# Performance work log

Hardware: AMD Instinct MI355X
Metric: run time of the kernel (lower is better)

## Reference

```python
import jax, jax.numpy as jnp
import numpy as np

B, N, XD = 4, 8192, 256   # batch, seq len, input/kv feature dim
F, H = 512, 8             # features, heads
D = F // H                # per-head dim = 64
EPS = 1e-6                # flax LayerNorm default epsilon


def _layer_norm(t, scale, bias):
    mu = jnp.mean(t, axis=-1, keepdims=True)
    var = jnp.mean(jnp.square(t - mu), axis=-1, keepdims=True)
    return (t - mu) * jax.lax.rsqrt(var + EPS) * scale + bias


def setup_inputs() -> dict:
    key = jax.random.key(0)
    ks = jax.random.split(key, 5)
    return {
        "x": jax.random.normal(ks[0], (B, N, XD), jnp.float32),
        "kv": jax.random.normal(ks[1], (B, N, XD), jnp.float32),
        # linen.initializers.normal(1/x_dim) / normal(1/h_dim)
        "Q": jax.random.normal(ks[2], (XD, F), jnp.float32) * (1.0 / XD),
        "K": jax.random.normal(ks[3], (XD, F), jnp.float32) * (1.0 / XD),
        "V": jax.random.normal(ks[4], (XD, F), jnp.float32) * (1.0 / XD),
        "log_scale": jnp.zeros((F,), jnp.float32),
        "ln_q_scale": jnp.ones((D,), jnp.float32),
        "ln_q_bias": jnp.zeros((D,), jnp.float32),
        "ln_k_scale": jnp.ones((D,), jnp.float32),
        "ln_k_bias": jnp.zeros((D,), jnp.float32),
        "ln_v_scale": jnp.ones((D,), jnp.float32),
        "ln_v_bias": jnp.zeros((D,), jnp.float32),
    }


def reference(x, kv, Q, K, V, log_scale,
              ln_q_scale, ln_q_bias, ln_k_scale, ln_k_bias, ln_v_scale, ln_v_bias):
    # QKV projections (value scaled by exp(log_scale) per feature)
    query = x @ Q                                    # [B, N, F]
    key = kv @ K                                     # [B, N, F]
    value = jnp.exp(log_scale) * (kv @ V)            # [B, N, F]
    # reshape exactly as the source module does
    q = query.reshape(B, H, -1, D)                   # [B, H, N, D]
    k = key.reshape(B, H, -1, D)
    v = value.reshape(B, H, -1, D)
    # per-head LayerNorm over the head dim (layer_norm=True)
    q = _layer_norm(q, ln_q_scale, ln_q_bias)
    k = _layer_norm(k, ln_k_scale, ln_k_bias)
    v = _layer_norm(v, ln_v_scale, ln_v_bias)
    # galerkin linear attention: Q @ (K^T V) / seq_len, no softmax, no NxN scores
    seq_len = k.shape[-2]
    ctx = jnp.einsum('bhnd,bhne->bhde', k, v)        # [B, H, D, D]
    out = jnp.einsum('bhnd,bhde->bhne', q, ctx) / seq_len
    return out.reshape(B, N, F)
```

## Files before the change

kernel.cpp:

```cpp
#include <hip/hip_runtime.h>
#include <stdint.h>

using f32x4  = __attribute__((ext_vector_type(4))) float;
using short8 = __attribute__((ext_vector_type(8))) short;
using u16x4  = __attribute__((ext_vector_type(4))) unsigned short;

#define MFMA(a, b, c) __builtin_amdgcn_mfma_f32_16x16x32_bf16((a), (b), (c), 0, 0, 0)

#define XDIM 256
#define FDIM 512
#define EPS  1e-6f

#define QT_OFF    0u
#define KT_OFF    262144u
#define VT_OFF    524288u
#define CTXT_OFF  786432u
#define PART_OFF  1048576u

static __device__ __forceinline__ unsigned short f2bf(float f) {
  unsigned u = __float_as_uint(f);
  unsigned r = u + 0x7FFFu + ((u >> 16) & 1u);
  return (unsigned short)(r >> 16);
}

static __device__ __forceinline__ void stage_a_full(const float* a_rows, int tid, char* Alds) {
  const int r = tid >> 2, cq = tid & 3;
  const float* src = a_rows + (size_t)r * XDIM + cq * 64;
  char* dst = Alds + r * 528 + cq * 128;
#pragma unroll
  for (int i = 0; i < 4; ++i) {
    float4 f0 = *(const float4*)(src + i * 16);
    float4 f1 = *(const float4*)(src + i * 16 + 4);
    float4 f2 = *(const float4*)(src + i * 16 + 8);
    float4 f3 = *(const float4*)(src + i * 16 + 12);
    short8 v0, v1;
    v0[0] = (short)f2bf(f0.x); v0[1] = (short)f2bf(f0.y);
    v0[2] = (short)f2bf(f0.z); v0[3] = (short)f2bf(f0.w);
    v0[4] = (short)f2bf(f1.x); v0[5] = (short)f2bf(f1.y);
    v0[6] = (short)f2bf(f1.z); v0[7] = (short)f2bf(f1.w);
    v1[0] = (short)f2bf(f2.x); v1[1] = (short)f2bf(f2.y);
    v1[2] = (short)f2bf(f2.z); v1[3] = (short)f2bf(f2.w);
    v1[4] = (short)f2bf(f3.x); v1[5] = (short)f2bf(f3.y);
    v1[6] = (short)f2bf(f3.z); v1[7] = (short)f2bf(f3.w);
    *(short8*)(dst + i * 32)      = v0;
    *(short8*)(dst + i * 32 + 16) = v1;
  }
}

static __device__ __forceinline__ void load_bphase(const char* base, int ks, int lr, int koff,
                                                   short8 b[8]) {
#pragma unroll
  for (int nt = 0; nt < 4; ++nt) {
    const char* r = base + (size_t)(nt * 16 + lr) * 512 + ks * 128 + koff;
    b[nt * 2]     = *(const short8*)(r);
    b[nt * 2 + 1] = *(const short8*)(r + 64);
  }
}

static __device__ __forceinline__ void chunk_layernorm(f32x4 acc[4][4], const float* sc,
                                                       const float* bs, int lane) {
  const int lr = lane & 15;
  float scl[4], bia[4];
#pragma unroll
  for (int nt = 0; nt < 4; ++nt) { scl[nt] = sc[nt * 16 + lr]; bia[nt] = bs[nt * 16 + lr]; }
#pragma unroll
  for (int mt = 0; mt < 4; ++mt) {
#pragma unroll
    for (int j = 0; j < 4; ++j) {
      float a0 = acc[mt][0][j], a1 = acc[mt][1][j], a2 = acc[mt][2][j], a3 = acc[mt][3][j];
      float s  = a0 + a1 + a2 + a3;
      float s2 = a0 * a0 + a1 * a1 + a2 * a2 + a3 * a3;
#pragma unroll
      for (int off = 1; off < 16; off <<= 1) {
        s  += __shfl_xor(s, off, 16);
        s2 += __shfl_xor(s2, off, 16);
      }
      const float mu  = s * (1.0f / 64.0f);
      const float var = s2 * (1.0f / 64.0f) - mu * mu;
      const float rs  = rsqrtf(var + EPS);
#pragma unroll
      for (int nt = 0; nt < 4; ++nt)
        acc[mt][nt][j] = (acc[mt][nt][j] - mu) * rs * scl[nt] + bia[nt];
    }
  }
}

__global__ void prep_weights_kernel(const float* __restrict__ Q, const float* __restrict__ K,
                                    const float* __restrict__ V, const float* __restrict__ ls,
                                    unsigned short* __restrict__ Qt, unsigned short* __restrict__ Kt,
                                    unsigned short* __restrict__ Vt) {
  const int flat = blockIdx.x * 256 + threadIdx.x;
  const int mat = flat >> 17;
  const int rem = flat & 131071;
  const int f = rem & 511;
  const int k = rem >> 9;
  if (mat == 0)      Qt[f * 256 + k] = f2bf(Q[k * 512 + f]);
  else if (mat == 1) Kt[f * 256 + k] = f2bf(K[k * 512 + f]);
  else               Vt[f * 256 + k] = f2bf(V[k * 512 + f] * expf(ls[f]));
}

__launch_bounds__(256, 2)
__global__ void kv_ctx_kernel(const float* __restrict__ kv,
                              const unsigned short* __restrict__ Kt,
                              const unsigned short* __restrict__ Vt,
                              const float* __restrict__ lnk_s, const float* __restrict__ lnk_b,
                              const float* __restrict__ lnv_s, const float* __restrict__ lnv_b,
                              float* __restrict__ partials) {
  __shared__ __align__(16) char smem[33792];

  const int tid = threadIdx.x, lane = tid & 63, w = tid >> 6;
  const int bid = blockIdx.x, rb = bid >> 1, nb = bid & 1;
  const int row0 = rb * 64;
  const int lr = lane & 15, lk = lane >> 4;
  const int koff = lk * 16;

  stage_a_full(kv + (size_t)row0 * XDIM, tid, smem);

  const f32x4 z4 = {0.f, 0.f, 0.f, 0.f};
  f32x4 acck[4][4], accv[4][4];
#pragma unroll
  for (int i = 0; i < 4; ++i)
#pragma unroll
    for (int j = 0; j < 4; ++j) { acck[i][j] = z4; accv[i][j] = z4; }

  const char* kbase = (const char*)Kt + (size_t)(nb * 256 + w * 64) * 512;
  const char* vbase = (const char*)Vt + (size_t)(nb * 256 + w * 64) * 512;

  short8 bufK[8], bufV[8];
  load_bphase(kbase, 0, lr, koff, bufK);
  load_bphase(vbase, 0, lr, koff, bufV);

  __syncthreads();

#pragma unroll
  for (int ks = 0; ks < 4; ++ks) {
    short8 a0[4], a1[4];
#pragma unroll
    for (int mt = 0; mt < 4; ++mt) {
      const char* ar = smem + (mt * 16 + lr) * 528 + ks * 128;
      a0[mt] = *(const short8*)(ar + koff);
      a1[mt] = *(const short8*)(ar + 64 + koff);
    }
#pragma unroll
    for (int mt = 0; mt < 4; ++mt)
#pragma unroll
      for (int nt = 0; nt < 4; ++nt) {
        acck[mt][nt] = MFMA(a0[mt], bufK[nt * 2],     acck[mt][nt]);
        acck[mt][nt] = MFMA(a1[mt], bufK[nt * 2 + 1], acck[mt][nt]);
      }
    if (ks < 3) load_bphase(kbase, ks + 1, lr, koff, bufK);
#pragma unroll
    for (int mt = 0; mt < 4; ++mt)
#pragma unroll
      for (int nt = 0; nt < 4; ++nt) {
        accv[mt][nt] = MFMA(a0[mt], bufV[nt * 2],     accv[mt][nt]);
        accv[mt][nt] = MFMA(a1[mt], bufV[nt * 2 + 1], accv[mt][nt]);
      }
    if (ks < 3) load_bphase(vbase, ks + 1, lr, koff, bufV);
  }

  chunk_layernorm(acck, lnk_s, lnk_b, lane);
  chunk_layernorm(accv, lnv_s, lnv_b, lane);

  char* knT = smem;
  char* vnT = smem + 16384;
  f32x4 cacc[4];
#pragma unroll
  for (int i = 0; i < 4; ++i) cacc[i] = z4;
  const int drow = w * 16 + lr;

#pragma unroll
  for (int half = 0; half < 2; ++half) {
    __syncthreads();
    if ((w >> 1) == half) {
      const int tb2 = (w & 1) * 128;
#pragma unroll
      for (int mt = 0; mt < 4; ++mt) {
        const int tb = tb2 + mt * 32 + lk * 8;
#pragma unroll
        for (int nt = 0; nt < 4; ++nt) {
          const int d = nt * 16 + lr;
          u16x4 pk, pv;
#pragma unroll
          for (int j = 0; j < 4; ++j) {
            pk[j] = f2bf(acck[mt][nt][j]);
            pv[j] = f2bf(accv[mt][nt][j]);
          }
          const int boff = d * 256 + (tb ^ ((d & 7) << 4));
          *(u16x4*)(knT + boff) = pk;
          *(u16x4*)(vnT + boff) = pv;
        }
      }
    }
    __syncthreads();
#pragma unroll
    for (int s = 0; s < 4; ++s) {
      const short8 a = *(const short8*)(knT + drow * 256 + ((s * 64 + koff) ^ ((drow & 7) << 4)));
#pragma unroll
      for (int nt = 0; nt < 4; ++nt) {
        const int e = nt * 16 + lr;
        const short8 b = *(const short8*)(vnT + e * 256 + ((s * 64 + koff) ^ ((e & 7) << 4)));
        cacc[nt] = MFMA(a, b, cacc[nt]);
      }
    }
  }

  float* pout = partials + (size_t)bid * 4096;
#pragma unroll
  for (int nt = 0; nt < 4; ++nt)
#pragma unroll
    for (int j = 0; j < 4; ++j)
      pout[(w * 16 + lk * 4 + j) * 64 + nt * 16 + lr] = cacc[nt][j];
}

__global__ void reduce_ctx_kernel(const float* __restrict__ partials,
                                  unsigned short* __restrict__ ctxTg) {
  const int bid = blockIdx.x, t = threadIdx.x;
  const int gg = bid >> 3, sl = bid & 7;
  const float* base = partials + (size_t)gg * 32 * 4096;
#pragma unroll
  for (int rep = 0; rep < 2; ++rep) {
    const int idx = sl * 512 + rep * 256 + t;
    float acc = 0.f;
#pragma unroll 8
    for (int p = 0; p < 32; ++p) acc += base[(size_t)p * 4096 + idx];
    const int d = idx >> 6, e = idx & 63;
    ctxTg[(size_t)gg * 4096 + e * 64 + d] = f2bf(acc * (1.0f / 8192.0f));
  }
}

__launch_bounds__(256, 2)
__global__ void q_out_kernel(const float* __restrict__ x, const unsigned short* __restrict__ Qt,
                             const unsigned short* __restrict__ ctxTg,
                             const float* __restrict__ lnq_s, const float* __restrict__ lnq_b,
                             float* __restrict__ out) {
  __shared__ __align__(16) char smem[43008];

  const int tid = threadIdx.x, lane = tid & 63, w = tid >> 6;
  const int bid = blockIdx.x, rb = bid >> 1, nb = bid & 1;
  const int row0 = rb * 64;
  const int g = row0 >> 10;
  const int lr = lane & 15, lk = lane >> 4;
  const int koff = lk * 16;
  char* ctxT = smem + 33792;

  stage_a_full(x + (size_t)row0 * XDIM, tid, smem);

  {
    const unsigned short* src = ctxTg + (size_t)g * 4096 + (tid >> 2) * 64 + (tid & 3) * 16;
    char* dst = ctxT + (tid >> 2) * 144 + (tid & 3) * 32;
    *(short8*)dst        = *(const short8*)(src);
    *(short8*)(dst + 16) = *(const short8*)(src + 8);
  }

  const f32x4 z4 = {0.f, 0.f, 0.f, 0.f};
  f32x4 acc[4][4];
#pragma unroll
  for (int i = 0; i < 4; ++i)
#pragma unroll
    for (int j = 0; j < 4; ++j) acc[i][j] = z4;

  const char* qbase = (const char*)Qt + (size_t)(nb * 256 + w * 64) * 512;

  short8 buf0[8], buf1[8];
  load_bphase(qbase, 0, lr, koff, buf0);

  __syncthreads();

#pragma unroll
  for (int ks = 0; ks < 4; ++ks) {
    if (ks == 0) load_bphase(qbase, 1, lr, koff, buf1);
    if (ks == 1) load_bphase(qbase, 2, lr, koff, buf0);
    if (ks == 2) load_bphase(qbase, 3, lr, koff, buf1);
    short8 a0[4], a1[4];
#pragma unroll
    for (int mt = 0; mt < 4; ++mt) {
      const char* ar = smem + (mt * 16 + lr) * 528 + ks * 128;
      a0[mt] = *(const short8*)(ar + koff);
      a1[mt] = *(const short8*)(ar + 64 + koff);
    }
#pragma unroll
    for (int mt = 0; mt < 4; ++mt)
#pragma unroll
      for (int nt = 0; nt < 4; ++nt) {
        if ((ks & 1) == 0) {
          acc[mt][nt] = MFMA(a0[mt], buf0[nt * 2],     acc[mt][nt]);
          acc[mt][nt] = MFMA(a1[mt], buf0[nt * 2 + 1], acc[mt][nt]);
        } else {
          acc[mt][nt] = MFMA(a0[mt], buf1[nt * 2],     acc[mt][nt]);
          acc[mt][nt] = MFMA(a1[mt], buf1[nt * 2 + 1], acc[mt][nt]);
        }
      }
  }

  chunk_layernorm(acc, lnq_s, lnq_b, lane);

  __syncthreads();

  char* A2 = smem + w * 8192;
#pragma unroll
  for (int mt = 0; mt < 4; ++mt)
#pragma unroll
    for (int j = 0; j < 4; ++j) {
      const int m = mt * 16 + lk * 4 + j;
      const int sw = (m & 7) << 4;
#pragma unroll
      for (int nt = 0; nt < 4; ++nt) {
        const int d = nt * 16 + lr;
        *(unsigned short*)(A2 + m * 128 + ((d * 2) ^ sw)) = f2bf(acc[mt][nt][j]);
      }
    }
  __syncthreads();

  f32x4 o[4][4];
#pragma unroll
  for (int i = 0; i < 4; ++i)
#pragma unroll
    for (int j = 0; j < 4; ++j) o[i][j] = z4;

#pragma unroll
  for (int s = 0; s < 2; ++s) {
    short8 a[4], b[4];
#pragma unroll
    for (int mt = 0; mt < 4; ++mt) {
      const int m = mt * 16 + lr;
      a[mt] = *(const short8*)(A2 + m * 128 + ((s * 64 + koff) ^ ((m & 7) << 4)));
    }
#pragma unroll
    for (int nt = 0; nt < 4; ++nt)
      b[nt] = *(const short8*)(ctxT + (nt * 16 + lr) * 144 + s * 64 + koff);
#pragma unroll
    for (int mt = 0; mt < 4; ++mt)
#pragma unroll
      for (int nt = 0; nt < 4; ++nt)
        o[mt][nt] = MFMA(a[mt], b[nt], o[mt][nt]);
  }

#pragma unroll
  for (int mt = 0; mt < 4; ++mt)
#pragma unroll
    for (int nt = 0; nt < 4; ++nt)
#pragma unroll
      for (int j = 0; j < 4; ++j) {
        const int n = mt * 16 + lk * 4 + j;
        out[(size_t)(row0 + n) * FDIM + nb * 256 + w * 64 + nt * 16 + lr] = o[mt][nt][j];
      }
}

extern "C" void kernel_launch(void* const* d_in, const int* in_sizes, int n_in,
                              void* d_out, int out_size, void* d_ws, size_t ws_size,
                              hipStream_t stream) {
  (void)in_sizes; (void)n_in; (void)out_size; (void)ws_size;
  const float* x     = (const float*)d_in[0];
  const float* kv    = (const float*)d_in[1];
  const float* Q     = (const float*)d_in[2];
  const float* K     = (const float*)d_in[3];
  const float* V     = (const float*)d_in[4];
  const float* ls    = (const float*)d_in[5];
  const float* lnq_s = (const float*)d_in[6];
  const float* lnq_b = (const float*)d_in[7];
  const float* lnk_s = (const float*)d_in[8];
  const float* lnk_b = (const float*)d_in[9];
  const float* lnv_s = (const float*)d_in[10];
  const float* lnv_b = (const float*)d_in[11];
  float* out = (float*)d_out;

  char* ws = (char*)d_ws;
  unsigned short* Qt   = (unsigned short*)(ws + QT_OFF);
  unsigned short* Kt   = (unsigned short*)(ws + KT_OFF);
  unsigned short* Vt   = (unsigned short*)(ws + VT_OFF);
  unsigned short* ctxT = (unsigned short*)(ws + CTXT_OFF);
  float* partials      = (float*)(ws + PART_OFF);

  prep_weights_kernel<<<1536, 256, 0, stream>>>(Q, K, V, ls, Qt, Kt, Vt);
  kv_ctx_kernel<<<1024, 256, 0, stream>>>(kv, Kt, Vt, lnk_s, lnk_b, lnv_s, lnv_b, partials);
  reduce_ctx_kernel<<<256, 256, 0, stream>>>(partials, ctxT);
  q_out_kernel<<<1024, 256, 0, stream>>>(x, Qt, ctxT, lnq_s, lnq_b, out);
}
```

Before: 109.9 us.

## Pre-convert kv to bf16, replace partial reduction with atomics, remap block order

kv is now converted to bf16 in a combined prep kernel, so kv_ctx reads A fragments straight from global memory without LDS staging or a barrier. The separate reduce kernel is removed. Each block instead atomically adds its context partial into a zeroed fp32 ctx buffer, and q_out scales and transposes it into LDS itself. Block-index remapping groups the two feature halves of nearby row blocks, likely for cache locality. In exchange this adds an extra bf16 round-trip of kv through memory, a memset, atomic contention, and non-deterministic summation order.

```diff
diff --git a/kernel.cpp b/kernel.cpp
--- a/kernel.cpp
+++ b/kernel.cpp
@@ -11,11 +11,11 @@
 #define FDIM 512
 #define EPS  1e-6f
 
-#define QT_OFF    0u
-#define KT_OFF    262144u
-#define VT_OFF    524288u
-#define CTXT_OFF  786432u
-#define PART_OFF  1048576u
+#define QT_OFF   0u
+#define KT_OFF   262144u
+#define VT_OFF   524288u
+#define CTX_OFF  786432u
+#define KVB_OFF  1310720u
 
 static __device__ __forceinline__ unsigned short f2bf(float f) {
   unsigned u = __float_as_uint(f);
@@ -23,16 +23,58 @@
   return (unsigned short)(r >> 16);
 }
 
-static __device__ __forceinline__ void stage_a_full(const float* a_rows, int tid, char* Alds) {
-  const int r = tid >> 2, cq = tid & 3;
-  const float* src = a_rows + (size_t)r * XDIM + cq * 64;
-  char* dst = Alds + r * 528 + cq * 128;
-#pragma unroll
-  for (int i = 0; i < 4; ++i) {
-    float4 f0 = *(const float4*)(src + i * 16);
-    float4 f1 = *(const float4*)(src + i * 16 + 4);
-    float4 f2 = *(const float4*)(src + i * 16 + 8);
-    float4 f3 = *(const float4*)(src + i * 16 + 12);
+static __device__ __forceinline__ void load_bphase(const char* base, int ks, int lr, int koff,
+                                                   short8 b[8]) {
+#pragma unroll
+  for (int nt = 0; nt < 4; ++nt) {
+    const char* r = base + (size_t)(nt * 16 + lr) * 512 + ks * 128 + koff;
+    b[nt * 2]     = *(const short8*)(r);
+    b[nt * 2 + 1] = *(const short8*)(r + 64);
+  }
+}
+
+static __device__ __forceinline__ void chunk_layernorm(f32x4 acc[4][4], const float* sc,
+                                                       const float* bs, int lane) {
+  const int lr = lane & 15;
+  float scl[4], bia[4];
+#pragma unroll
+  for (int nt = 0; nt < 4; ++nt) { scl[nt] = sc[nt * 16 + lr]; bia[nt] = bs[nt * 16 + lr]; }
+#pragma unroll
+  for (int mt = 0; mt < 4; ++mt) {
+#pragma unroll
+    for (int j = 0; j < 4; ++j) {
+      float a0 = acc[mt][0][j], a1 = acc[mt][1][j], a2 = acc[mt][2][j], a3 = acc[mt][3][j];
+      float s  = a0 + a1 + a2 + a3;
+      float s2 = a0 * a0 + a1 * a1 + a2 * a2 + a3 * a3;
+#pragma unroll
+      for (int off = 1; off < 16; off <<= 1) {
+        s  += __shfl_xor(s, off, 16);
+        s2 += __shfl_xor(s2, off, 16);
+      }
+      const float mu  = s * (1.0f / 64.0f);
+      const float var = s2 * (1.0f / 64.0f) - mu * mu;
+      const float rs  = rsqrtf(var + EPS);
+#pragma unroll
+      for (int nt = 0; nt < 4; ++nt)
+        acc[mt][nt][j] = (acc[mt][nt][j] - mu) * rs * scl[nt] + bia[nt];
+    }
+  }
+}
+
+__global__ void prep_kernel(const float* __restrict__ kv,
+                            const float* __restrict__ Q, const float* __restrict__ K,
+                            const float* __restrict__ V, const float* __restrict__ ls,
+                            unsigned short* __restrict__ kvb,
+                            unsigned short* __restrict__ Qt, unsigned short* __restrict__ Kt,
+                            unsigned short* __restrict__ Vt) {
+  const int bid = blockIdx.x, tid = threadIdx.x;
+  if (bid < 2048) {
+    const size_t base = ((size_t)bid * 256 + tid) * 16;
+    const float* src = kv + base;
+    float4 f0 = *(const float4*)(src);
+    float4 f1 = *(const float4*)(src + 4);
+    float4 f2 = *(const float4*)(src + 8);
+    float4 f3 = *(const float4*)(src + 12);
     short8 v0, v1;
     v0[0] = (short)f2bf(f0.x); v0[1] = (short)f2bf(f0.y);
     v0[2] = (short)f2bf(f0.z); v0[3] = (short)f2bf(f0.w);
@@ -42,80 +84,38 @@
     v1[2] = (short)f2bf(f2.z); v1[3] = (short)f2bf(f2.w);
     v1[4] = (short)f2bf(f3.x); v1[5] = (short)f2bf(f3.y);
     v1[6] = (short)f2bf(f3.z); v1[7] = (short)f2bf(f3.w);
-    *(short8*)(dst + i * 32)      = v0;
-    *(short8*)(dst + i * 32 + 16) = v1;
-  }
-}
-
-static __device__ __forceinline__ void load_bphase(const char* base, int ks, int lr, int koff,
-                                                   short8 b[8]) {
-#pragma unroll
-  for (int nt = 0; nt < 4; ++nt) {
-    const char* r = base + (size_t)(nt * 16 + lr) * 512 + ks * 128 + koff;
-    b[nt * 2]     = *(const short8*)(r);
-    b[nt * 2 + 1] = *(const short8*)(r + 64);
-  }
-}
-
-static __device__ __forceinline__ void chunk_layernorm(f32x4 acc[4][4], const float* sc,
-                                                       const float* bs, int lane) {
-  const int lr = lane & 15;
-  float scl[4], bia[4];
-#pragma unroll
-  for (int nt = 0; nt < 4; ++nt) { scl[nt] = sc[nt * 16 + lr]; bia[nt] = bs[nt * 16 + lr]; }
-#pragma unroll
-  for (int mt = 0; mt < 4; ++mt) {
-#pragma unroll
-    for (int j = 0; j < 4; ++j) {
-      float a0 = acc[mt][0][j], a1 = acc[mt][1][j], a2 = acc[mt][2][j], a3 = acc[mt][3][j];
-      float s  = a0 + a1 + a2 + a3;
-      float s2 = a0 * a0 + a1 * a1 + a2 * a2 + a3 * a3;
-#pragma unroll
-      for (int off = 1; off < 16; off <<= 1) {
-        s  += __shfl_xor(s, off, 16);
-        s2 += __shfl_xor(s2, off, 16);
-      }
-      const float mu  = s * (1.0f / 64.0f);
-      const float var = s2 * (1.0f / 64.0f) - mu * mu;
-      const float rs  = rsqrtf(var + EPS);
-#pragma unroll
-      for (int nt = 0; nt < 4; ++nt)
-        acc[mt][nt][j] = (acc[mt][nt][j] - mu) * rs * scl[nt] + bia[nt];
-    }
-  }
-}
-
-__global__ void prep_weights_kernel(const float* __restrict__ Q, const float* __restrict__ K,
-                                    const float* __restrict__ V, const float* __restrict__ ls,
-                                    unsigned short* __restrict__ Qt, unsigned short* __restrict__ Kt,
-                                    unsigned short* __restrict__ Vt) {
-  const int flat = blockIdx.x * 256 + threadIdx.x;
-  const int mat = flat >> 17;
-  const int rem = flat & 131071;
-  const int f = rem & 511;
-  const int k = rem >> 9;
-  if (mat == 0)      Qt[f * 256 + k] = f2bf(Q[k * 512 + f]);
-  else if (mat == 1) Kt[f * 256 + k] = f2bf(K[k * 512 + f]);
-  else               Vt[f * 256 + k] = f2bf(V[k * 512 + f] * expf(ls[f]));
+    *(short8*)(kvb + base)     = v0;
+    *(short8*)(kvb + base + 8) = v1;
+  } else {
+    const int flat = (bid - 2048) * 256 + tid;
+    const int mat = flat >> 17;
+    const int rem = flat & 131071;
+    const int f = rem & 511;
+    const int k = rem >> 9;
+    if (mat == 0)      Qt[f * 256 + k] = f2bf(Q[k * 512 + f]);
+    else if (mat == 1) Kt[f * 256 + k] = f2bf(K[k * 512 + f]);
+    else               Vt[f * 256 + k] = f2bf(V[k * 512 + f] * expf(ls[f]));
+  }
 }
 
 __launch_bounds__(256, 2)
-__global__ void kv_ctx_kernel(const float* __restrict__ kv,
+__global__ void kv_ctx_kernel(const unsigned short* __restrict__ kvb,
                               const unsigned short* __restrict__ Kt,
                               const unsigned short* __restrict__ Vt,
                               const float* __restrict__ lnk_s, const float* __restrict__ lnk_b,
                               const float* __restrict__ lnv_s, const float* __restrict__ lnv_b,
-                              float* __restrict__ partials) {
-  __shared__ __align__(16) char smem[33792];
+                              float* __restrict__ ctx) {
+  __shared__ __align__(16) char smem[32768];
 
   const int tid = threadIdx.x, lane = tid & 63, w = tid >> 6;
-  const int bid = blockIdx.x, rb = bid >> 1, nb = bid & 1;
+  const int bid = blockIdx.x;
+  const int rb = ((bid >> 4) << 3) | (bid & 7);
+  const int nb = (bid >> 3) & 1;
   const int row0 = rb * 64;
+  const int g = row0 >> 10;
   const int lr = lane & 15, lk = lane >> 4;
   const int koff = lk * 16;
 
-  stage_a_full(kv + (size_t)row0 * XDIM, tid, smem);
-
   const f32x4 z4 = {0.f, 0.f, 0.f, 0.f};
   f32x4 acck[4][4], accv[4][4];
 #pragma unroll
@@ -123,6 +123,7 @@
 #pragma unroll
     for (int j = 0; j < 4; ++j) { acck[i][j] = z4; accv[i][j] = z4; }
 
+  const char* abase = (const char*)kvb + (size_t)row0 * 512;
   const char* kbase = (const char*)Kt + (size_t)(nb * 256 + w * 64) * 512;
   const char* vbase = (const char*)Vt + (size_t)(nb * 256 + w * 64) * 512;
 
@@ -130,16 +131,14 @@
   load_bphase(kbase, 0, lr, koff, bufK);
   load_bphase(vbase, 0, lr, koff, bufV);
 
-  __syncthreads();
-
 #pragma unroll
   for (int ks = 0; ks < 4; ++ks) {
     short8 a0[4], a1[4];
 #pragma unroll
     for (int mt = 0; mt < 4; ++mt) {
-      const char* ar = smem + (mt * 16 + lr) * 528 + ks * 128;
-      a0[mt] = *(const short8*)(ar + koff);
-      a1[mt] = *(const short8*)(ar + 64 + koff);
+      const char* ar = abase + (size_t)(mt * 16 + lr) * 512 + ks * 128 + koff;
+      a0[mt] = *(const short8*)(ar);
+      a1[mt] = *(const short8*)(ar + 64);
     }
 #pragma unroll
     for (int mt = 0; mt < 4; ++mt)
@@ -205,52 +204,63 @@
     }
   }
 
-  float* pout = partials + (size_t)bid * 4096;
+  float* cdst = ctx + (size_t)g * 4096;
 #pragma unroll
   for (int nt = 0; nt < 4; ++nt)
 #pragma unroll
     for (int j = 0; j < 4; ++j)
-      pout[(w * 16 + lk * 4 + j) * 64 + nt * 16 + lr] = cacc[nt][j];
-}
-
-__global__ void reduce_ctx_kernel(const float* __restrict__ partials,
-                                  unsigned short* __restrict__ ctxTg) {
-  const int bid = blockIdx.x, t = threadIdx.x;
-  const int gg = bid >> 3, sl = bid & 7;
-  const float* base = partials + (size_t)gg * 32 * 4096;
-#pragma unroll
-  for (int rep = 0; rep < 2; ++rep) {
-    const int idx = sl * 512 + rep * 256 + t;
-    float acc = 0.f;
-#pragma unroll 8
-    for (int p = 0; p < 32; ++p) acc += base[(size_t)p * 4096 + idx];
-    const int d = idx >> 6, e = idx & 63;
-    ctxTg[(size_t)gg * 4096 + e * 64 + d] = f2bf(acc * (1.0f / 8192.0f));
-  }
+      atomicAdd(cdst + (w * 16 + lk * 4 + j) * 64 + nt * 16 + lr, cacc[nt][j]);
 }
 
 __launch_bounds__(256, 2)
 __global__ void q_out_kernel(const float* __restrict__ x, const unsigned short* __restrict__ Qt,
-                             const unsigned short* __restrict__ ctxTg,
+                             const float* __restrict__ ctx,
                              const float* __restrict__ lnq_s, const float* __restrict__ lnq_b,
                              float* __restrict__ out) {
   __shared__ __align__(16) char smem[43008];
 
   const int tid = threadIdx.x, lane = tid & 63, w = tid >> 6;
-  const int bid = blockIdx.x, rb = bid >> 1, nb = bid & 1;
+  const int bid = blockIdx.x;
+  const int rb = ((bid >> 4) << 3) | (bid & 7);
+  const int nb = (bid >> 3) & 1;
   const int row0 = rb * 64;
   const int g = row0 >> 10;
   const int lr = lane & 15, lk = lane >> 4;
   const int koff = lk * 16;
   char* ctxT = smem + 33792;
 
-  stage_a_full(x + (size_t)row0 * XDIM, tid, smem);
-
   {
-    const unsigned short* src = ctxTg + (size_t)g * 4096 + (tid >> 2) * 64 + (tid & 3) * 16;
-    char* dst = ctxT + (tid >> 2) * 144 + (tid & 3) * 32;
-    *(short8*)dst        = *(const short8*)(src);
-    *(short8*)(dst + 16) = *(const short8*)(src + 8);
+    const int r = tid >> 2, cq = tid & 3;
+    const float* src = x + (size_t)(row0 + r) * XDIM + cq * 64;
+    char* dst = smem + r * 528 + cq * 128;
+#pragma unroll
+    for (int i = 0; i < 4; ++i) {
+      float4 f0 = *(const float4*)(src + i * 16);
+      float4 f1 = *(const float4*)(src + i * 16 + 4);
+      float4 f2 = *(const float4*)(src + i * 16 + 8);
+      float4 f3 = *(const float4*)(src + i * 16 + 12);
+      short8 v0, v1;
+      v0[0] = (short)f2bf(f0.x); v0[1] = (short)f2bf(f0.y);
+      v0[2] = (short)f2bf(f0.z); v0[3] = (short)f2bf(f0.w);
+      v0[4] = (short)f2bf(f1.x); v0[5] = (short)f2bf(f1.y);
+      v0[6] = (short)f2bf(f1.z); v0[7] = (short)f2bf(f1.w);
+      v1[0] = (short)f2bf(f2.x); v1[1] = (short)f2bf(f2.y);
+      v1[2] = (short)f2bf(f2.z); v1[3] = (short)f2bf(f2.w);
+      v1[4] = (short)f2bf(f3.x); v1[5] = (short)f2bf(f3.y);
+      v1[6] = (short)f2bf(f3.z); v1[7] = (short)f2bf(f3.w);
+      *(short8*)(dst + i * 32)      = v0;
+      *(short8*)(dst + i * 32 + 16) = v1;
+    }
+  }
+
+  {
+    const int d = tid >> 2, e0 = (tid & 3) * 16;
+    const float* csrc = ctx + (size_t)g * 4096 + d * 64 + e0;
+#pragma unroll
+    for (int i = 0; i < 16; ++i) {
+      const unsigned short v = f2bf(csrc[i] * (1.0f / 8192.0f));
+      *(unsigned short*)(ctxT + (e0 + i) * 144 + d * 2) = v;
+    }
   }
 
   const f32x4 z4 = {0.f, 0.f, 0.f, 0.f};
@@ -366,14 +376,14 @@
   float* out = (float*)d_out;
 
   char* ws = (char*)d_ws;
-  unsigned short* Qt   = (unsigned short*)(ws + QT_OFF);
-  unsigned short* Kt   = (unsigned short*)(ws + KT_OFF);
-  unsigned short* Vt   = (unsigned short*)(ws + VT_OFF);
-  unsigned short* ctxT = (unsigned short*)(ws + CTXT_OFF);
-  float* partials      = (float*)(ws + PART_OFF);
-
-  prep_weights_kernel<<<1536, 256, 0, stream>>>(Q, K, V, ls, Qt, Kt, Vt);
-  kv_ctx_kernel<<<1024, 256, 0, stream>>>(kv, Kt, Vt, lnk_s, lnk_b, lnv_s, lnv_b, partials);
-  reduce_ctx_kernel<<<256, 256, 0, stream>>>(partials, ctxT);
-  q_out_kernel<<<1024, 256, 0, stream>>>(x, Qt, ctxT, lnq_s, lnq_b, out);
-}
+  unsigned short* Qt  = (unsigned short*)(ws + QT_OFF);
+  unsigned short* Kt  = (unsigned short*)(ws + KT_OFF);
+  unsigned short* Vt  = (unsigned short*)(ws + VT_OFF);
+  float* ctx          = (float*)(ws + CTX_OFF);
+  unsigned short* kvb = (unsigned short*)(ws + KVB_OFF);
+
+  hipMemsetAsync(ws + CTX_OFF, 0, 32 * 4096 * sizeof(float), stream);
+  prep_kernel<<<3584, 256, 0, stream>>>(kv, Q, K, V, ls, kvb, Qt, Kt, Vt);
+  kv_ctx_kernel<<<1024, 256, 0, stream>>>(kvb, Kt, Vt, lnk_s, lnk_b, lnv_s, lnv_b, ctx);
+  q_out_kernel<<<1024, 256, 0, stream>>>(x, Qt, ctx, lnq_s, lnq_b, out);
+}
```

Result: slower. 128.4 us (+16.8%).
